# Performance work log

Measured on AMD Instinct MI355X. Metric: run time of the kernel, lower is better.

## Reference

```python
import jax, jax.numpy as jnp
import numpy as np

B, T, C, H, E, L = 4, 1024, 768, 12, 4, 2
DH = C // H


def setup_inputs() -> dict:
    key = jax.random.key(0)
    ks = jax.random.split(key, 10)
    s = 0.02  # init scale; keeps unscaled-attention logits sane (source has no 1/sqrt(d))
    w = lambda k, shape: (jax.random.normal(k, shape, jnp.float32) * s)
    z = lambda shape: jnp.zeros(shape, jnp.float32)
    return dict(
        x=jax.random.normal(ks[0], (B, T, C), jnp.float32),
        gate_W=w(ks[1], (C, E)), gate_b=z((E,)),
        Wq=w(ks[2], (E, L, C, C)), bq=z((E, L, C)),
        Wk=w(ks[3], (E, L, C, C)), bk=z((E, L, C)),
        Wv=w(ks[4], (E, L, C, C)), bv=z((E, L, C)),
        Wo=w(ks[5], (E, L, C, C)), bo=z((E, L, C)),
        ln_g=jnp.ones((E, L, C), jnp.float32), ln_b=z((E, L, C)),
        Wfc=w(ks[6], (E, L, C, 4 * C)), bfc=z((E, L, 4 * C)),
        Wpr=w(ks[7], (E, L, 4 * C, C)), bpr=z((E, L, C)),
    )


def _attn(x, Wq, bq, Wk, bk, Wv, bv, Wo, bo):
    # FlashAttention3 blockwise loop == exact full softmax(Q K^T) V, NO scaling, NO mask
    q = (x @ Wq + bq).reshape(B, T, H, DH)
    k = (x @ Wk + bk).reshape(B, T, H, DH)
    v = (x @ Wv + bv).reshape(B, T, H, DH)
    s = jnp.einsum('bqhd,bkhd->bhqk', q, k)
    p = jax.nn.softmax(s, axis=-1)
    o = jnp.einsum('bhqk,bkhd->bqhd', p, v).reshape(B, T, C)
    return o @ Wo + bo


def _ln(x, g, b, eps=1e-5):
    m = x.mean(-1, keepdims=True)
    v = ((x - m) ** 2).mean(-1, keepdims=True)
    return (x - m) * jax.lax.rsqrt(v + eps) * g + b


def _expert(x, Wq, bq, Wk, bk, Wv, bv, Wo, bo, ln_g, ln_b, Wfc, bfc, Wpr, bpr):
    # Sequential(attn, layernorm, mlp) x L — no residuals, dropout=0 (eval)
    for l in range(L):
        x = _attn(x, Wq[l], bq[l], Wk[l], bk[l], Wv[l], bv[l], Wo[l], bo[l])
        x = _ln(x, ln_g[l], ln_b[l])
        h = jax.nn.gelu(x @ Wfc[l] + bfc[l], approximate=True)  # tanh GELU
        x = h @ Wpr[l] + bpr[l]
    return x


def reference(x, gate_W, gate_b, Wq, bq, Wk, bk, Wv, bv, Wo, bo,
              ln_g, ln_b, Wfc, bfc, Wpr, bpr):
    gate_probs = jax.nn.softmax(x @ gate_W + gate_b, axis=-1)  # [B,T,E]
    expert_fn = jax.vmap(_expert, in_axes=(None,) + (0,) * 14)
    eo = expert_fn(x, Wq, bq, Wk, bk, Wv, bv, Wo, bo, ln_g, ln_b, Wfc, bfc, Wpr, bpr)  # [E,B,T,C]
    return jnp.einsum('bte,ebtc->btc', gate_probs, eo)
```

## Files before the change

### kernel.cpp

```cpp
#include <hip/hip_runtime.h>

#define B_ 4
#define T_ 1024
#define C_ 768
#define H_ 12
#define E_ 4
#define L_ 2
#define DH_ 64
#define M_ (B_*T_)
#define LOG2E_ 1.4426950408889634f

typedef __attribute__((ext_vector_type(8))) short bf16x8;
typedef __attribute__((ext_vector_type(4))) float f32x4;

__device__ __forceinline__ unsigned short f2bf(float f) {
  unsigned int u = __float_as_uint(f);
  unsigned int r = (u + 0x7FFFu + ((u >> 16) & 1u)) >> 16;
  return (unsigned short)r;
}
__device__ __forceinline__ float bf2f(unsigned short s) {
  return __uint_as_float(((unsigned int)s) << 16);
}
__device__ __forceinline__ unsigned int cvt_pk_bf16(float lo, float hi) {
  unsigned int r;
  asm("v_cvt_pk_bf16_f32 %0, %1, %2" : "=v"(r) : "v"(lo), "v"(hi));
  return r;
}

typedef __attribute__((address_space(1))) unsigned int gu32;
typedef __attribute__((address_space(3))) unsigned int lu32;
__device__ __forceinline__ void gld_lds16(const void* g, void* l) {
  __builtin_amdgcn_global_load_lds((gu32*)g, (lu32*)l, 16, 0, 0);
}

__device__ __forceinline__ float gelu_fast(float x) {
  float u = 0.7978845608028654f * x * (1.0f + 0.044715f * x * x);
  float d = 1.0f + exp2f(-2.8853900817779268f * u);
  return x * __builtin_amdgcn_rcpf(d);
}

template <int ACT>
__global__ __launch_bounds__(256) void gemm_bt(
    const unsigned short* __restrict__ A, const unsigned short* __restrict__ Bt,
    const float* __restrict__ bias, unsigned short* __restrict__ D,
    int M, int N, int K, long long sA, long long sB, long long sBias, long long sD,
    float bscale)
{
  __shared__ unsigned short shA[2][128*32];
  __shared__ unsigned short shB[2][128*32];
  const int tid = threadIdx.x;
  const int wid = tid >> 6, lane = tid & 63;
  const int l15 = lane & 15, lhi = lane >> 4;
  const int wr = wid >> 1, wc = wid & 1;
  const int m0 = blockIdx.y * 128, n0 = blockIdx.x * 128;
  const int g = blockIdx.z;
  const unsigned short* Ab = A + (size_t)g * sA;
  const unsigned short* Bb = Bt + (size_t)g * sB;
  const float* biasb = bias + (size_t)g * sBias;
  unsigned short* Db = D + (size_t)g * sD;

  f32x4 acc[4][4] = {};
  const int qq = (tid & 7) ^ ((tid >> 3) & 7);
  const int srow = ((tid >> 3) << 1) + (qq >> 2);
  const int schk = (qq & 3) << 3;

  const int half64 = l15 >> 1;
  const int slot = (((((l15 & 1) << 2) | lhi) ^ (half64 & 7)) << 3);

  auto stage = [&](int buf, int k0) {
    #pragma unroll
    for (int p = 0; p < 2; ++p) {
      gld_lds16(Ab + (size_t)(m0 + p*64 + srow) * K + (k0 + schk), &shA[buf][(p*256 + wid*64)*8]);
      gld_lds16(Bb + (size_t)(n0 + p*64 + srow) * K + (k0 + schk), &shB[buf][(p*256 + wid*64)*8]);
    }
  };
  auto compute = [&](int buf) {
    bf16x8 af[4], bfr[4];
    #pragma unroll
    for (int i = 0; i < 4; ++i)
      af[i] = *(const bf16x8*)&shA[buf][(wr*32 + i*8 + half64)*64 + slot];
    #pragma unroll
    for (int j = 0; j < 4; ++j)
      bfr[j] = *(const bf16x8*)&shB[buf][(wc*32 + j*8 + half64)*64 + slot];
    #pragma unroll
    for (int i = 0; i < 4; ++i)
      #pragma unroll
      for (int j = 0; j < 4; ++j)
        acc[i][j] = __builtin_amdgcn_mfma_f32_16x16x32_bf16(af[i], bfr[j], acc[i][j], 0, 0, 0);
  };

  stage(0, 0);
  stage(1, 32);
  int cur = 0;

  int k0 = 0;
  for (; k0 < K - 64; k0 += 32) {
    asm volatile("s_waitcnt vmcnt(4)" ::: "memory");
    __builtin_amdgcn_s_barrier();
    compute(cur);
    __builtin_amdgcn_s_barrier();
    stage(cur, k0 + 64);
    cur ^= 1;
  }
  asm volatile("s_waitcnt vmcnt(4)" ::: "memory");
  __builtin_amdgcn_s_barrier();
  compute(cur);
  cur ^= 1;
  asm volatile("s_waitcnt vmcnt(0)" ::: "memory");
  __builtin_amdgcn_s_barrier();
  compute(cur);

  #pragma unroll
  for (int j = 0; j < 4; ++j) {
    const int col = n0 + wc*64 + j*16 + l15;
    const float bv = bscale * biasb[col];
    #pragma unroll
    for (int i = 0; i < 4; ++i) {
      const int r0 = m0 + wr*64 + i*16 + lhi*4;
      #pragma unroll
      for (int r = 0; r < 4; ++r) {
        float v = acc[i][j][r] + bv;
        if (ACT == 1) v = gelu_fast(v);
        Db[(size_t)(r0 + r) * N + col] = f2bf(v);
      }
    }
  }
}

__global__ __launch_bounds__(256) void flash_attn(
    const unsigned short* __restrict__ q, const unsigned short* __restrict__ k,
    const unsigned short* __restrict__ vt, unsigned short* __restrict__ o)
{
  __shared__ unsigned short shK[2][64*64];
  __shared__ unsigned short shV[2][64*64];
  __shared__ unsigned short shP[4][16*64];
  const int tid = threadIdx.x;
  const int wid = tid >> 6, lane = tid & 63;
  const int l15 = lane & 15, lhi = lane >> 4;
  const int qt = blockIdx.x, h = blockIdx.y, eb = blockIdx.z;

  const unsigned short* qrow = q + ((size_t)eb*T_ + qt*64 + wid*16 + l15) * C_ + h*DH_;
  bf16x8 aq0 = *(const bf16x8*)(qrow + lhi*8);
  bf16x8 aq1 = *(const bf16x8*)(qrow + 32 + lhi*8);

  f32x4 oacc[4] = {};
  float mrun = -1e30f, lpart = 0.f;

  const int krow = tid >> 3;
  const int swzsrc = (((tid & 7) ^ (krow & 7)) << 3);
  const unsigned short* kbase = k + ((size_t)eb*T_)*C_ + h*DH_;
  const unsigned short* vbase = vt + ((size_t)eb*H_ + h)*DH_*T_;

  auto stage = [&](int buf, int kt) {
    #pragma unroll
    for (int p = 0; p < 2; ++p) {
      gld_lds16(kbase + (size_t)(kt*64 + krow + p*32)*C_ + swzsrc,
                &shK[buf][(p*256 + wid*64)*8]);
      gld_lds16(vbase + (size_t)(krow + p*32)*T_ + kt*64 + swzsrc,
                &shV[buf][(p*256 + wid*64)*8]);
    }
  };

  stage(0, 0);
  __syncthreads();
  int cur = 0;
  const int swzr = l15 & 7;
  const int c0 = (lhi ^ swzr) << 3;
  const int c1 = ((4 + lhi) ^ swzr) << 3;
  const int pwbase = l15*64 + ((lhi & 1) << 2);
  const int pwh = lhi >> 1;

  for (int kt = 0; kt < T_/64; ++kt) {
    if (kt + 1 < T_/64) stage(cur ^ 1, kt + 1);

    f32x4 s[4];
    #pragma unroll
    for (int kb = 0; kb < 4; ++kb) {
      const int row = (kb*16 + l15)*64;
      bf16x8 bk0 = *(const bf16x8*)&shK[cur][row + c0];
      bf16x8 bk1 = *(const bf16x8*)&shK[cur][row + c1];
      f32x4 z = {};
      z = __builtin_amdgcn_mfma_f32_16x16x32_bf16(bk0, aq0, z, 0, 0, 0);
      s[kb] = __builtin_amdgcn_mfma_f32_16x16x32_bf16(bk1, aq1, z, 0, 0, 0);
    }
    float mt = fmaxf(fmaxf(s[0][0], s[0][1]), fmaxf(s[0][2], s[0][3]));
    #pragma unroll
    for (int kb = 1; kb < 4; ++kb)
      mt = fmaxf(mt, fmaxf(fmaxf(s[kb][0], s[kb][1]), fmaxf(s[kb][2], s[kb][3])));
    mt = fmaxf(mt, __shfl_xor(mt, 16));
    mt = fmaxf(mt, __shfl_xor(mt, 32));

    if (__any(mt - mrun > 8.0f)) {
      float mnew = fmaxf(mrun, mt);
      float sc = exp2f(mrun - mnew);
      mrun = mnew;
      lpart *= sc;
      #pragma unroll
      for (int r = 0; r < 4; ++r) {
        float scr = __shfl(sc, lhi*4 + r);
        #pragma unroll
        for (int n = 0; n < 4; ++n) oacc[n][r] *= scr;
      }
    }
    unsigned int pk0[4], pk1[4];
    #pragma unroll
    for (int kb = 0; kb < 4; ++kb) {
      #pragma unroll
      for (int r = 0; r < 4; ++r) {
        float pv = exp2f(s[kb][r] - mrun);
        s[kb][r] = pv;
        lpart += pv;
      }
      pk0[kb] = cvt_pk_bf16(s[kb][0], s[kb][1]);
      pk1[kb] = cvt_pk_bf16(s[kb][2], s[kb][3]);
    }
    #pragma unroll
    for (int kb = 0; kb < 4; ++kb) {
      const int chunk = (2*kb + pwh) ^ swzr;
      uint2 w = {pk0[kb], pk1[kb]};
      *(uint2*)&shP[wid][pwbase + chunk*8] = w;
    }
    bf16x8 pa0 = *(const bf16x8*)&shP[wid][l15*64 + c0];
    bf16x8 pa1 = *(const bf16x8*)&shP[wid][l15*64 + c1];
    #pragma unroll
    for (int n = 0; n < 4; ++n) {
      const int row = (n*16 + l15)*64;
      bf16x8 bv0 = *(const bf16x8*)&shV[cur][row + c0];
      bf16x8 bv1 = *(const bf16x8*)&shV[cur][row + c1];
      oacc[n] = __builtin_amdgcn_mfma_f32_16x16x32_bf16(pa0, bv0, oacc[n], 0, 0, 0);
      oacc[n] = __builtin_amdgcn_mfma_f32_16x16x32_bf16(pa1, bv1, oacc[n], 0, 0, 0);
    }
    __syncthreads();
    cur ^= 1;
  }
  lpart += __shfl_xor(lpart, 16);
  lpart += __shfl_xor(lpart, 32);
  float li[4];
  #pragma unroll
  for (int r = 0; r < 4; ++r) li[r] = __shfl(lpart, lhi*4 + r);
  #pragma unroll
  for (int n = 0; n < 4; ++n)
    #pragma unroll
    for (int r = 0; r < 4; ++r) {
      float v = oacc[n][r] / li[r];
      o[((size_t)eb*T_ + qt*64 + wid*16 + lhi*4 + r) * C_ + h*DH_ + n*16 + l15] = f2bf(v);
    }
}

__global__ void transpose_cast(const float* __restrict__ in, unsigned short* __restrict__ out,
                               int K, int N, long long inStride, long long outStride, float scale)
{
  __shared__ float tile[32][33];
  const float* src = in + (size_t)blockIdx.z * inStride;
  unsigned short* dst = out + (size_t)blockIdx.z * outStride;
  const int tx = threadIdx.x, ty = threadIdx.y;
  const int k0 = blockIdx.y*32, n0 = blockIdx.x*32;
  #pragma unroll
  for (int j = 0; j < 32; j += 8)
    tile[ty+j][tx] = src[(size_t)(k0+ty+j)*N + n0+tx];
  __syncthreads();
  #pragma unroll
  for (int j = 0; j < 32; j += 8)
    dst[(size_t)(n0+ty+j)*K + k0+tx] = f2bf(scale * tile[tx][ty+j]);
}

__global__ void transpose_v_kernel(const unsigned short* __restrict__ v, unsigned short* __restrict__ vt)
{
  __shared__ unsigned short tile[32][33];
  const int t0 = blockIdx.x * 32, d0 = blockIdx.y * 32;
  const int z = blockIdx.z;
  const int h = z % H_, eb = z / H_;
  const int tx = threadIdx.x, ty = threadIdx.y;
  #pragma unroll
  for (int j = 0; j < 32; j += 8)
    tile[ty+j][tx] = v[((size_t)eb*T_ + t0+ty+j)*C_ + h*DH_ + d0 + tx];
  __syncthreads();
  #pragma unroll
  for (int j = 0; j < 32; j += 8)
    vt[((size_t)z*DH_ + d0+ty+j)*T_ + t0 + tx] = tile[tx][ty+j];
}

__global__ __launch_bounds__(256) void ln_kernel(
    const unsigned short* __restrict__ in, unsigned short* __restrict__ out,
    const float* __restrict__ g, const float* __restrict__ b)
{
  const int row = blockIdx.x * 4 + (threadIdx.x >> 6);
  const int lane = threadIdx.x & 63;
  const int e = row >> 12;
  const unsigned short* ir = in + (size_t)row * C_;
  unsigned short* orow = out + (size_t)row * C_;
  const float* gg = g + (size_t)e * (L_*C_);
  const float* bb = b + (size_t)e * (L_*C_);
  float v[12]; float s = 0.f, s2 = 0.f;
  #pragma unroll
  for (int j = 0; j < 12; ++j) {
    float x = bf2f(ir[lane + 64*j]);
    v[j] = x; s += x; s2 += x*x;
  }
  #pragma unroll
  for (int d = 32; d; d >>= 1) { s += __shfl_xor(s, d); s2 += __shfl_xor(s2, d); }
  float mean = s * (1.f/C_);
  float var = s2 * (1.f/C_) - mean*mean;
  float rstd = rsqrtf(var + 1e-5f);
  #pragma unroll
  for (int j = 0; j < 12; ++j) {
    int c = lane + 64*j;
    orow[c] = f2bf((v[j]-mean)*rstd*gg[c] + bb[c]);
  }
}

__global__ __launch_bounds__(256) void gate_kernel(
    const float* __restrict__ x, const float* __restrict__ gw, const float* __restrict__ gb,
    float* __restrict__ gp)
{
  const int row = blockIdx.x * 4 + (threadIdx.x >> 6);
  const int lane = threadIdx.x & 63;
  const float* xr = x + (size_t)row * C_;
  float a0=0.f, a1=0.f, a2=0.f, a3=0.f;
  for (int i = lane; i < C_; i += 64) {
    float xv = xr[i];
    float4 w = ((const float4*)gw)[i];
    a0 += xv*w.x; a1 += xv*w.y; a2 += xv*w.z; a3 += xv*w.w;
  }
  #pragma unroll
  for (int d = 32; d; d >>= 1) {
    a0 += __shfl_xor(a0,d); a1 += __shfl_xor(a1,d);
    a2 += __shfl_xor(a2,d); a3 += __shfl_xor(a3,d);
  }
  if (lane == 0) {
    a0 += gb[0]; a1 += gb[1]; a2 += gb[2]; a3 += gb[3];
    float m = fmaxf(fmaxf(a0,a1), fmaxf(a2,a3));
    float e0 = __expf(a0-m), e1 = __expf(a1-m), e2 = __expf(a2-m), e3 = __expf(a3-m);
    float inv = 1.f/(e0+e1+e2+e3);
    float4 r = {e0*inv, e1*inv, e2*inv, e3*inv};
    ((float4*)gp)[row] = r;
  }
}

__global__ __launch_bounds__(256) void cast_x_kernel(const float* __restrict__ x,
                                                     unsigned short* __restrict__ xbf)
{
  const size_t i = (size_t)blockIdx.x * 256 + threadIdx.x;
  float4 v = ((const float4*)x)[i];
  ushort4 u;
  u.x = f2bf(v.x); u.y = f2bf(v.y); u.z = f2bf(v.z); u.w = f2bf(v.w);
  #pragma unroll
  for (int e = 0; e < E_; ++e)
    ((ushort4*)(xbf + (size_t)e * ((size_t)M_*C_)))[i] = u;
}

__global__ __launch_bounds__(256) void combine_kernel(
    const unsigned short* __restrict__ xbf, const float* __restrict__ gp, float* __restrict__ out)
{
  const size_t i = (size_t)blockIdx.x * 256 + threadIdx.x;
  const int row = (int)((i*4) / C_);
  float4 gpv = ((const float4*)gp)[row];
  const float* gpf = (const float*)&gpv;
  float r0=0.f, r1=0.f, r2=0.f, r3=0.f;
  #pragma unroll
  for (int e = 0; e < E_; ++e) {
    ushort4 u = ((const ushort4*)(xbf + (size_t)e*((size_t)M_*C_)))[i];
    float ge = gpf[e];
    r0 += ge*bf2f(u.x); r1 += ge*bf2f(u.y); r2 += ge*bf2f(u.z); r3 += ge*bf2f(u.w);
  }
  float4 res = {r0, r1, r2, r3};
  ((float4*)out)[i] = res;
}

extern "C" void kernel_launch(void* const* d_in, const int* in_sizes, int n_in,
                              void* d_out, int out_size, void* d_ws, size_t ws_size,
                              hipStream_t stream) {
  const float* x      = (const float*)d_in[0];
  const float* gate_W = (const float*)d_in[1];
  const float* gate_b = (const float*)d_in[2];
  const float* Wq = (const float*)d_in[3];
  const float* bq = (const float*)d_in[4];
  const float* Wk = (const float*)d_in[5];
  const float* bk = (const float*)d_in[6];
  const float* Wv = (const float*)d_in[7];
  const float* bv = (const float*)d_in[8];
  const float* Wo = (const float*)d_in[9];
  const float* bo = (const float*)d_in[10];
  const float* ln_g = (const float*)d_in[11];
  const float* ln_b = (const float*)d_in[12];
  const float* Wfc = (const float*)d_in[13];
  const float* bfc = (const float*)d_in[14];
  const float* Wpr = (const float*)d_in[15];
  const float* bpr = (const float*)d_in[16];
  float* out = (float*)d_out;

  const size_t CC  = (size_t)C_*C_;
  const size_t C4C = (size_t)C_*4*C_;
  const size_t MC  = (size_t)M_*C_;
  const size_t M4C = (size_t)M_*4*C_;

  char* p = (char*)d_ws;
  auto carve = [&](size_t bytes) { char* r = p; p += (bytes + 255) & ~(size_t)255; return r; };
  unsigned short* wqT  = (unsigned short*)carve(E_*CC*2);
  unsigned short* wkT  = (unsigned short*)carve(E_*CC*2);
  unsigned short* wvT  = (unsigned short*)carve(E_*CC*2);
  unsigned short* woT  = (unsigned short*)carve(E_*CC*2);
  unsigned short* wfcT = (unsigned short*)carve(E_*C4C*2);
  unsigned short* wprT = (unsigned short*)carve(E_*C4C*2);
  unsigned short* xbf  = (unsigned short*)carve(E_*MC*2);
  unsigned short* r1   = (unsigned short*)carve((size_t)4*E_*MC*2);
  float* gp = (float*)carve((size_t)M_*E_*4);

  unsigned short* qb  = r1;
  unsigned short* kb  = r1 + (size_t)E_*MC;
  unsigned short* vb  = r1 + (size_t)2*E_*MC;
  unsigned short* vtb = r1 + (size_t)3*E_*MC;
  unsigned short* ob  = vb;
  unsigned short* tb  = vtb;
  unsigned short* hb  = r1;

  dim3 blk256(256);
  dim3 blkT(32, 8);

  cast_x_kernel<<<dim3((unsigned)(MC/4/256)), blk256, 0, stream>>>(x, xbf);
  gate_kernel<<<dim3(M_/4), blk256, 0, stream>>>(x, gate_W, gate_b, gp);

  for (int l = 0; l < L_; ++l) {
    transpose_cast<<<dim3(24,24,E_), blkT, 0, stream>>>(Wq + l*CC,  wqT,  C_,   C_,   (long long)(L_*CC),  (long long)CC, LOG2E_);
    transpose_cast<<<dim3(24,24,E_), blkT, 0, stream>>>(Wk + l*CC,  wkT,  C_,   C_,   (long long)(L_*CC),  (long long)CC, 1.0f);
    transpose_cast<<<dim3(24,24,E_), blkT, 0, stream>>>(Wv + l*CC,  wvT,  C_,   C_,   (long long)(L_*CC),  (long long)CC, 1.0f);
    transpose_cast<<<dim3(24,24,E_), blkT, 0, stream>>>(Wo + l*CC,  woT,  C_,   C_,   (long long)(L_*CC),  (long long)CC, 1.0f);
    transpose_cast<<<dim3(96,24,E_), blkT, 0, stream>>>(Wfc + l*C4C, wfcT, C_,   4*C_, (long long)(L_*C4C), (long long)C4C, 1.0f);
    transpose_cast<<<dim3(24,96,E_), blkT, 0, stream>>>(Wpr + l*C4C, wprT, 4*C_, C_,   (long long)(L_*C4C), (long long)C4C, 1.0f);

    gemm_bt<0><<<dim3(C_/128, M_/128, E_), blk256, 0, stream>>>(
        xbf, wqT, bq + l*C_, qb, M_, C_, C_, (long long)MC, (long long)CC, (long long)(L_*C_), (long long)MC, LOG2E_);
    gemm_bt<0><<<dim3(C_/128, M_/128, E_), blk256, 0, stream>>>(
        xbf, wkT, bk + l*C_, kb, M_, C_, C_, (long long)MC, (long long)CC, (long long)(L_*C_), (long long)MC, 1.0f);
    gemm_bt<0><<<dim3(C_/128, M_/128, E_), blk256, 0, stream>>>(
        xbf, wvT, bv + l*C_, vb, M_, C_, C_, (long long)MC, (long long)CC, (long long)(L_*C_), (long long)MC, 1.0f);

    transpose_v_kernel<<<dim3(T_/32, DH_/32, E_*B_*H_), blkT, 0, stream>>>(vb, vtb);
    flash_attn<<<dim3(T_/64, H_, E_*B_), blk256, 0, stream>>>(qb, kb, vtb, ob);

    gemm_bt<0><<<dim3(C_/128, M_/128, E_), blk256, 0, stream>>>(
        ob, woT, bo + l*C_, tb, M_, C_, C_, (long long)MC, (long long)CC, (long long)(L_*C_), (long long)MC, 1.0f);

    ln_kernel<<<dim3(E_*M_/4), blk256, 0, stream>>>(tb, xbf, ln_g + l*C_, ln_b + l*C_);

    gemm_bt<1><<<dim3(4*C_/128, M_/128, E_), blk256, 0, stream>>>(
        xbf, wfcT, bfc + l*4*C_, hb, M_, 4*C_, C_, (long long)MC, (long long)C4C, (long long)(L_*4*C_), (long long)M4C, 1.0f);
    gemm_bt<0><<<dim3(C_/128, M_/128, E_), blk256, 0, stream>>>(
        hb, wprT, bpr + l*C_, xbf, M_, C_, 4*C_, (long long)M4C, (long long)C4C, (long long)(L_*C_), (long long)MC, 1.0f);
  }

  combine_kernel<<<dim3((unsigned)(MC/4/256)), blk256, 0, stream>>>(xbf, gp, out);
}
```

Before: 1.114 ms.

## Replace 128x128 GEMM with 256x256x64 tile, 512-thread kernel

Replaces the batched bf16 GEMM with a larger 256x256 output tile and a 64-deep K step using 8 warps, a new XOR-swizzled LDS layout, and s_setprio around MFMA bursts. The aim is to raise arithmetic intensity and cut global/LDS traffic per FLOP. In exchange, the 768-wide GEMMs launch only 192 blocks, and each block needs 128 KB of LDS, which limits occupancy and tail utilization.

Measured after the change: 1.060 ms. -4.8%, faster.

```diff
diff --git a/kernel.cpp b/kernel.cpp
--- a/kernel.cpp
+++ b/kernel.cpp
@@ -40,86 +40,96 @@
 }
 
 template <int ACT>
-__global__ __launch_bounds__(256) void gemm_bt(
+__global__ __launch_bounds__(512, 2) void gemm256(
     const unsigned short* __restrict__ A, const unsigned short* __restrict__ Bt,
     const float* __restrict__ bias, unsigned short* __restrict__ D,
     int M, int N, int K, long long sA, long long sB, long long sBias, long long sD,
     float bscale)
 {
-  __shared__ unsigned short shA[2][128*32];
-  __shared__ unsigned short shB[2][128*32];
+  __shared__ unsigned short shA[2][256*64];
+  __shared__ unsigned short shB[2][256*64];
   const int tid = threadIdx.x;
-  const int wid = tid >> 6, lane = tid & 63;
+  const int lane = tid & 63, wid = tid >> 6;
   const int l15 = lane & 15, lhi = lane >> 4;
-  const int wr = wid >> 1, wc = wid & 1;
-  const int m0 = blockIdx.y * 128, n0 = blockIdx.x * 128;
+  const int wm = wid >> 2, wn = wid & 3;
+  const int m0 = blockIdx.y * 256, n0 = blockIdx.x * 256;
   const int g = blockIdx.z;
   const unsigned short* Ab = A + (size_t)g * sA;
   const unsigned short* Bb = Bt + (size_t)g * sB;
   const float* biasb = bias + (size_t)g * sBias;
   unsigned short* Db = D + (size_t)g * sD;
 
-  f32x4 acc[4][4] = {};
-  const int qq = (tid & 7) ^ ((tid >> 3) & 7);
-  const int srow = ((tid >> 3) << 1) + (qq >> 2);
-  const int schk = (qq & 3) << 3;
-
-  const int half64 = l15 >> 1;
-  const int slot = (((((l15 & 1) << 2) | lhi) ^ (half64 & 7)) << 3);
-
+  f32x4 acc[8][4] = {};
+
+  const int srow = tid >> 3;
+  const int schk = (((tid & 7) ^ (srow & 7)) << 3);
   auto stage = [&](int buf, int k0) {
     #pragma unroll
-    for (int p = 0; p < 2; ++p) {
-      gld_lds16(Ab + (size_t)(m0 + p*64 + srow) * K + (k0 + schk), &shA[buf][(p*256 + wid*64)*8]);
-      gld_lds16(Bb + (size_t)(n0 + p*64 + srow) * K + (k0 + schk), &shB[buf][(p*256 + wid*64)*8]);
-    }
+    for (int p = 0; p < 4; ++p)
+      gld_lds16(Ab + (size_t)(m0 + p*64 + srow) * K + (k0 + schk), &shA[buf][p*4096 + tid*8]);
+    #pragma unroll
+    for (int p = 0; p < 4; ++p)
+      gld_lds16(Bb + (size_t)(n0 + p*64 + srow) * K + (k0 + schk), &shB[buf][p*4096 + tid*8]);
   };
+
+  const int swz = l15 & 7;
+  const int ca0 = (lhi ^ swz) << 3;
+  const int ca1 = ((4 + lhi) ^ swz) << 3;
+
   auto compute = [&](int buf) {
-    bf16x8 af[4], bfr[4];
-    #pragma unroll
-    for (int i = 0; i < 4; ++i)
-      af[i] = *(const bf16x8*)&shA[buf][(wr*32 + i*8 + half64)*64 + slot];
-    #pragma unroll
-    for (int j = 0; j < 4; ++j)
-      bfr[j] = *(const bf16x8*)&shB[buf][(wc*32 + j*8 + half64)*64 + slot];
-    #pragma unroll
-    for (int i = 0; i < 4; ++i)
+    #pragma unroll
+    for (int kh = 0; kh < 2; ++kh) {
+      const int cc = kh ? ca1 : ca0;
+      bf16x8 bfrag[4];
       #pragma unroll
-      for (int j = 0; j < 4; ++j)
-        acc[i][j] = __builtin_amdgcn_mfma_f32_16x16x32_bf16(af[i], bfr[j], acc[i][j], 0, 0, 0);
+      for (int nf = 0; nf < 4; ++nf)
+        bfrag[nf] = *(const bf16x8*)&shB[buf][(wn*64 + nf*16 + l15)*64 + cc];
+      #pragma unroll
+      for (int mh = 0; mh < 2; ++mh) {
+        bf16x8 afr[4];
+        #pragma unroll
+        for (int i = 0; i < 4; ++i)
+          afr[i] = *(const bf16x8*)&shA[buf][(wm*128 + (mh*4 + i)*16 + l15)*64 + cc];
+        __builtin_amdgcn_s_setprio(1);
+        #pragma unroll
+        for (int i = 0; i < 4; ++i)
+          #pragma unroll
+          for (int nf = 0; nf < 4; ++nf)
+            acc[mh*4+i][nf] = __builtin_amdgcn_mfma_f32_16x16x32_bf16(
+                afr[i], bfrag[nf], acc[mh*4+i][nf], 0, 0, 0);
+        __builtin_amdgcn_s_setprio(0);
+      }
+    }
   };
 
+  const int nkt = K >> 6;
   stage(0, 0);
-  stage(1, 32);
-  int cur = 0;
-
-  int k0 = 0;
-  for (; k0 < K - 64; k0 += 32) {
-    asm volatile("s_waitcnt vmcnt(4)" ::: "memory");
+  stage(1, 64);
+
+  for (int kt = 0; kt < nkt - 2; ++kt) {
+    asm volatile("s_waitcnt vmcnt(8)" ::: "memory");
     __builtin_amdgcn_s_barrier();
-    compute(cur);
+    compute(kt & 1);
     __builtin_amdgcn_s_barrier();
-    stage(cur, k0 + 64);
-    cur ^= 1;
-  }
-  asm volatile("s_waitcnt vmcnt(4)" ::: "memory");
+    stage(kt & 1, (kt + 2) << 6);
+  }
+  asm volatile("s_waitcnt vmcnt(8)" ::: "memory");
   __builtin_amdgcn_s_barrier();
-  compute(cur);
-  cur ^= 1;
+  compute((nkt - 2) & 1);
   asm volatile("s_waitcnt vmcnt(0)" ::: "memory");
   __builtin_amdgcn_s_barrier();
-  compute(cur);
-
-  #pragma unroll
-  for (int j = 0; j < 4; ++j) {
-    const int col = n0 + wc*64 + j*16 + l15;
+  compute((nkt - 1) & 1);
+
+  #pragma unroll
+  for (int nf = 0; nf < 4; ++nf) {
+    const int col = n0 + wn*64 + nf*16 + l15;
     const float bv = bscale * biasb[col];
     #pragma unroll
-    for (int i = 0; i < 4; ++i) {
-      const int r0 = m0 + wr*64 + i*16 + lhi*4;
+    for (int mf = 0; mf < 8; ++mf) {
+      const int r0 = m0 + wm*128 + mf*16 + lhi*4;
       #pragma unroll
       for (int r = 0; r < 4; ++r) {
-        float v = acc[i][j][r] + bv;
+        float v = acc[mf][nf][r] + bv;
         if (ACT == 1) v = gelu_fast(v);
         Db[(size_t)(r0 + r) * N + col] = f2bf(v);
       }
@@ -415,6 +425,7 @@
   unsigned short* hb  = r1;
 
   dim3 blk256(256);
+  dim3 blk512(512);
   dim3 blkT(32, 8);
 
   cast_x_kernel<<<dim3((unsigned)(MC/4/256)), blk256, 0, stream>>>(x, xbf);
@@ -428,24 +439,24 @@
     transpose_cast<<<dim3(96,24,E_), blkT, 0, stream>>>(Wfc + l*C4C, wfcT, C_,   4*C_, (long long)(L_*C4C), (long long)C4C, 1.0f);
     transpose_cast<<<dim3(24,96,E_), blkT, 0, stream>>>(Wpr + l*C4C, wprT, 4*C_, C_,   (long long)(L_*C4C), (long long)C4C, 1.0f);
 
-    gemm_bt<0><<<dim3(C_/128, M_/128, E_), blk256, 0, stream>>>(
+    gemm256<0><<<dim3(C_/256, M_/256, E_), blk512, 0, stream>>>(
         xbf, wqT, bq + l*C_, qb, M_, C_, C_, (long long)MC, (long long)CC, (long long)(L_*C_), (long long)MC, LOG2E_);
-    gemm_bt<0><<<dim3(C_/128, M_/128, E_), blk256, 0, stream>>>(
+    gemm256<0><<<dim3(C_/256, M_/256, E_), blk512, 0, stream>>>(
         xbf, wkT, bk + l*C_, kb, M_, C_, C_, (long long)MC, (long long)CC, (long long)(L_*C_), (long long)MC, 1.0f);
-    gemm_bt<0><<<dim3(C_/128, M_/128, E_), blk256, 0, stream>>>(
+    gemm256<0><<<dim3(C_/256, M_/256, E_), blk512, 0, stream>>>(
         xbf, wvT, bv + l*C_, vb, M_, C_, C_, (long long)MC, (long long)CC, (long long)(L_*C_), (long long)MC, 1.0f);
 
     transpose_v_kernel<<<dim3(T_/32, DH_/32, E_*B_*H_), blkT, 0, stream>>>(vb, vtb);
     flash_attn<<<dim3(T_/64, H_, E_*B_), blk256, 0, stream>>>(qb, kb, vtb, ob);
 
-    gemm_bt<0><<<dim3(C_/128, M_/128, E_), blk256, 0, stream>>>(
+    gemm256<0><<<dim3(C_/256, M_/256, E_), blk512, 0, stream>>>(
         ob, woT, bo + l*C_, tb, M_, C_, C_, (long long)MC, (long long)CC, (long long)(L_*C_), (long long)MC, 1.0f);
 
     ln_kernel<<<dim3(E_*M_/4), blk256, 0, stream>>>(tb, xbf, ln_g + l*C_, ln_b + l*C_);
 
-    gemm_bt<1><<<dim3(4*C_/128, M_/128, E_), blk256, 0, stream>>>(
+    gemm256<1><<<dim3(4*C_/256, M_/256, E_), blk512, 0, stream>>>(
         xbf, wfcT, bfc + l*4*C_, hb, M_, 4*C_, C_, (long long)MC, (long long)C4C, (long long)(L_*4*C_), (long long)M4C, 1.0f);
-    gemm_bt<0><<<dim3(C_/128, M_/128, E_), blk256, 0, stream>>>(
+    gemm256<0><<<dim3(C_/256, M_/256, E_), blk512, 0, stream>>>(
         hb, wprT, bpr + l*C_, xbf, M_, C_, 4*C_, (long long)M4C, (long long)C4C, (long long)(L_*C_), (long long)MC, 1.0f);
   }
 
```
